# Kernel tuning notes

Hardware: AMD Instinct MI355X
Metric: run time of the kernel (lower is better)

Reference implementation:

```python
import jax, jax.numpy as jnp
import numpy as np

D_IN, HID, HEADS, MAXN, OUT, B = 16, 128, 4, 8, 128, 32768
HD = HID // HEADS
EPS = 1e-5


def _ln(x, g, b):
    m = jnp.mean(x, -1, keepdims=True)
    v = jnp.mean((x - m) ** 2, -1, keepdims=True)
    return (x - m) * jax.lax.rsqrt(v + EPS) * g + b


def _encode(x, enc_w1, enc_b1, enc_g1, enc_be1, enc_w2, enc_b2, enc_g2, enc_be2):
    h = _ln(x @ enc_w1.T + enc_b1, enc_g1, enc_be1)
    h = jax.nn.relu(h)
    return _ln(h @ enc_w2.T + enc_b2, enc_g2, enc_be2)


def setup_inputs() -> dict:
    key = jax.random.key(0)
    ks = jax.random.split(key, 12)

    def xavier(k, shape):
        # xavier_uniform with gain=0.5, matching _init_weights
        lim = 0.5 * np.sqrt(6.0 / (shape[0] + shape[1]))
        return jax.random.uniform(k, shape, jnp.float32, -lim, lim)

    z = lambda n: jnp.zeros((n,), jnp.float32)
    o = lambda n: jnp.ones((n,), jnp.float32)
    return {
        "current_node": jax.random.normal(ks[0], (B, D_IN), jnp.float32),
        "neighbor_nodes": jax.random.normal(ks[1], (B, MAXN, D_IN), jnp.float32),
        "neighbor_mask": jax.random.randint(ks[2], (B, MAXN), 0, 2, jnp.int32),
        "enc_w1": xavier(ks[3], (HID, D_IN)), "enc_b1": z(HID),
        "enc_g1": o(HID), "enc_be1": z(HID),
        "enc_w2": xavier(ks[4], (HID, HID)), "enc_b2": z(HID),
        "enc_g2": o(HID), "enc_be2": z(HID),
        "in_proj_w": xavier(ks[5], (3 * HID, HID)), "in_proj_b": z(3 * HID),
        "out_w": xavier(ks[6], (HID, HID)), "out_b": z(HID),
        "an_g": o(HID), "an_b": z(HID),
        "p1_w": xavier(ks[7], (HID, 2 * HID)), "p1_b": z(HID),
        "p1_g": o(HID), "p1_be": z(HID),
        "p2_w": xavier(ks[8], (OUT, HID)), "p2_b": z(OUT),
        "p2_g": o(OUT), "p2_be": z(OUT),
    }


def _forward(current_node, neighbor_nodes, neighbor_mask,
             enc_w1, enc_b1, enc_g1, enc_be1, enc_w2, enc_b2, enc_g2, enc_be2,
             in_proj_w, in_proj_b, out_w, out_b, an_g, an_b,
             p1_w, p1_b, p1_g, p1_be, p2_w, p2_b, p2_g, p2_be):
    bsz = current_node.shape[0]
    cur_emb = _encode(current_node, enc_w1, enc_b1, enc_g1, enc_be1,
                      enc_w2, enc_b2, enc_g2, enc_be2)                  # [B, HID]
    nb_emb = _encode(neighbor_nodes, enc_w1, enc_b1, enc_g1, enc_be1,
                     enc_w2, enc_b2, enc_g2, enc_be2)                   # [B, N, HID]

    valid = neighbor_mask > 0                                            # [B, N]
    has_nb = jnp.any(valid, axis=1)                                      # [B]

    # MultiheadAttention (eval mode, dropout inactive): q from current node, k/v from neighbors
    wq, wk, wv = in_proj_w[:HID], in_proj_w[HID:2 * HID], in_proj_w[2 * HID:]
    bq, bk, bv = in_proj_b[:HID], in_proj_b[HID:2 * HID], in_proj_b[2 * HID:]
    q = (cur_emb @ wq.T + bq).reshape(bsz, HEADS, HD)                    # [B, H, hd]
    k = (nb_emb @ wk.T + bk).reshape(bsz, MAXN, HEADS, HD)               # [B, N, H, hd]
    v = (nb_emb @ wv.T + bv).reshape(bsz, MAXN, HEADS, HD)

    scores = jnp.einsum('bhd,bnhd->bhn', q, k) / np.sqrt(HD)             # [B, H, N]
    # rows with zero valid neighbors get a fully-open mask to avoid NaN softmax;
    # their attention result is discarded below (replaced by cur_emb)
    safe = jnp.where(has_nb[:, None], valid, True)                       # [B, N]
    scores = jnp.where(safe[:, None, :], scores, -1e9)
    attn = jax.nn.softmax(scores, axis=-1)                               # [B, H, N]
    ctx = jnp.einsum('bhn,bnhd->bhd', attn, v).reshape(bsz, HID)
    ctx = ctx @ out_w.T + out_b
    agg = jnp.where(has_nb[:, None], _ln(ctx, an_g, an_b), cur_emb)      # [B, HID]

    combined = jnp.concatenate([cur_emb, agg], axis=-1)                  # [B, 2*HID]
    h = _ln(combined @ p1_w.T + p1_b, p1_g, p1_be)
    h = jax.nn.relu(h)
    return _ln(h @ p2_w.T + p2_b, p2_g, p2_be)                           # [B, OUT]


def reference(current_node, neighbor_nodes, neighbor_mask,
              enc_w1, enc_b1, enc_g1, enc_be1, enc_w2, enc_b2, enc_g2, enc_be2,
              in_proj_w, in_proj_b, out_w, out_b, an_g, an_b,
              p1_w, p1_b, p1_g, p1_be, p2_w, p2_b, p2_g, p2_be):
    return _forward(current_node, neighbor_nodes, neighbor_mask,
                    enc_w1, enc_b1, enc_g1, enc_be1, enc_w2, enc_b2, enc_g2, enc_be2,
                    in_proj_w, in_proj_b, out_w, out_b, an_g, an_b,
                    p1_w, p1_b, p1_g, p1_be, p2_w, p2_b, p2_g, p2_be)
```

## Files before the change

### kernel.cpp

```cpp
#include <hip/hip_runtime.h>

#define DEV __device__ __forceinline__

typedef __attribute__((ext_vector_type(8))) short bf16x8;
typedef __attribute__((ext_vector_type(4))) float f32x4;

static constexpr int NTH = 512;
static constexpr int TBE = 16;

static constexpr int W1P = 0;
static constexpr int W2  = 4096;
static constexpr int WQ  = 20480;
static constexpr int WK  = 36864;
static constexpr int WVW = 53248;
static constexpr int OW  = 69632;
static constexpr int P1A = 86016;
static constexpr int P1B = 102400;
static constexpr int P2W = 118784;
static constexpr int WS_BF16_TOT = 135168;
static constexpr int NPRM = 18 * 128;
static constexpr int WQr  = 139776;
static constexpr int OWr  = 156160;
static constexpr int P1Ar = 172544;
static constexpr int P1Br = 188928;
static constexpr int P2r  = 205312;
static constexpr int CURE = 221696;
static constexpr int NBE  = 221696 + 4194304;
static constexpr size_t SPLIT_NEED = (size_t)(NBE + 33554432) * 2;

DEV unsigned short f2bf(float f) {
  unsigned u = __float_as_uint(f);
  return (unsigned short)((u + 0x7fffu + ((u >> 16) & 1u)) >> 16);
}
DEV float bf2f(unsigned short u) { return __uint_as_float(((unsigned)u) << 16); }

DEV void st_bf16(unsigned short* buf, int row, int col, float v) {
  buf[row * 128 + ((((col >> 3) ^ (row & 7)) << 3) | (col & 7))] = f2bf(v);
}
DEV float ld_bf16(const unsigned short* buf, int row, int col) {
  unsigned u = buf[row * 128 + ((((col >> 3) ^ (row & 7)) << 3) | (col & 7))];
  return __uint_as_float(u << 16);
}
DEV bf16x8 frag128(const unsigned short* buf, int row, int kk, int lg) {
  return *(const bf16x8*)(buf + row * 128 + (((kk * 4 + lg) ^ (row & 7)) << 3));
}
DEV bf16x8 frag32(const unsigned short* buf, int row, int lg) {
  return *(const bf16x8*)(buf + row * 32 + ((lg ^ (row & 3)) << 3));
}
DEV f32x4 mfma16(bf16x8 a, bf16x8 b, f32x4 c) {
  return __builtin_amdgcn_mfma_f32_16x16x32_bf16(a, b, c, 0, 0, 0);
}

__global__ void prep(const float* __restrict__ enc_w1, const float* __restrict__ enc_w2,
                     const float* __restrict__ in_pw, const float* __restrict__ out_w,
                     const float* __restrict__ p1_w, const float* __restrict__ p2_w,
                     const float* __restrict__ enc_b1, const float* __restrict__ enc_g1,
                     const float* __restrict__ enc_be1, const float* __restrict__ enc_b2,
                     const float* __restrict__ enc_g2, const float* __restrict__ enc_be2,
                     const float* __restrict__ in_pb, const float* __restrict__ out_b,
                     const float* __restrict__ an_g, const float* __restrict__ an_b,
                     const float* __restrict__ p1_b, const float* __restrict__ p1_g,
                     const float* __restrict__ p1_be, const float* __restrict__ p2_b,
                     const float* __restrict__ p2_g, const float* __restrict__ p2_be,
                     unsigned short* __restrict__ wsb, float* __restrict__ wsp, int rm) {
  int t = blockIdx.x * blockDim.x + threadIdx.x;
  int NT = gridDim.x * blockDim.x;
  for (int i = t; i < 8 * 16384; i += NT) {
    int mi = i >> 14, e = i & 16383, row = e >> 7, col = e & 127;
    float v; int dstb;
    switch (mi) {
      case 0: v = enc_w2[row * 128 + col];         dstb = W2;  break;
      case 1: v = in_pw[row * 128 + col];          dstb = WQ;  break;
      case 2: v = in_pw[(128 + row) * 128 + col];  dstb = WK;  break;
      case 3: v = in_pw[(256 + row) * 128 + col];  dstb = WVW; break;
      case 4: v = out_w[row * 128 + col];          dstb = OW;  break;
      case 5: v = p1_w[row * 256 + col];           dstb = P1A; break;
      case 6: v = p1_w[row * 256 + 128 + col];     dstb = P1B; break;
      default: v = p2_w[row * 128 + col];          dstb = P2W; break;
    }
    wsb[dstb + row * 128 + ((((col >> 3) ^ (row & 7)) << 3) | (col & 7))] = f2bf(v);
  }
  for (int i = t; i < 4096; i += NT) {
    int row = i >> 5, col = i & 31;
    float v = (col < 16) ? enc_w1[row * 16 + col] : 0.f;
    wsb[W1P + row * 32 + ((((col >> 3) ^ (row & 3)) << 3) | (col & 7))] = f2bf(v);
  }
  if (rm) {
    for (int i = t; i < 5 * 16384; i += NT) {
      int mi = i >> 14, e = i & 16383, row = e >> 7, col = e & 127;
      float v; int dstb;
      switch (mi) {
        case 0: v = in_pw[row * 128 + col];         dstb = WQr;  break;
        case 1: v = out_w[row * 128 + col];         dstb = OWr;  break;
        case 2: v = p1_w[row * 256 + col];          dstb = P1Ar; break;
        case 3: v = p1_w[row * 256 + 128 + col];    dstb = P1Br; break;
        default: v = p2_w[row * 128 + col];         dstb = P2r;  break;
      }
      wsb[dstb + e] = f2bf(v);
    }
  }
  for (int i = t; i < NPRM; i += NT) {
    int s = i >> 7, c = i & 127; float v;
    switch (s) {
      case 0: v = enc_b1[c]; break;  case 1: v = enc_g1[c]; break;
      case 2: v = enc_be1[c]; break; case 3: v = enc_b2[c]; break;
      case 4: v = enc_g2[c]; break;  case 5: v = enc_be2[c]; break;
      case 6: v = in_pb[c]; break;   case 7: v = in_pb[128 + c]; break;
      case 8: v = in_pb[256 + c]; break; case 9: v = out_b[c]; break;
      case 10: v = an_g[c]; break;   case 11: v = an_b[c]; break;
      case 12: v = p1_b[c]; break;   case 13: v = p1_g[c]; break;
      case 14: v = p1_be[c]; break;  case 15: v = p2_b[c]; break;
      case 16: v = p2_g[c]; break;   default: v = p2_be[c]; break;
    }
    wsp[i] = v;
  }
}

__global__ __launch_bounds__(512, 4)
void k1_enc(const float* __restrict__ cur_x, const float* __restrict__ nb_x,
            const unsigned short* __restrict__ wsb, const float* __restrict__ wsp,
            unsigned short* __restrict__ wse) {
  __shared__ __align__(16) unsigned short s_w1[4096];
  __shared__ __align__(16) unsigned short s_w2[16384];
  __shared__ __align__(16) unsigned short s_h1[8][16 * 136];
  __shared__ float s_prm[6 * 128];

  const int tid = threadIdx.x;
  const int wv = tid >> 6, l = tid & 63, l15 = l & 15, lg = l >> 4;

  ((uint4*)s_w1)[tid] = ((const uint4*)(wsb + W1P))[tid];
#pragma unroll
  for (int i = 0; i < 4; ++i)
    ((uint4*)s_w2)[tid + i * 512] = ((const uint4*)(wsb + W2))[tid + i * 512];
  for (int i = tid; i < 768; i += 512) s_prm[i] = wsp[i];
  __syncthreads();

  unsigned short* h1 = &s_h1[wv][0];

  auto ln_t = [&](float (&acc)[8][4], int bs, int gs, int es, bool relu) {
#pragma unroll
    for (int ct = 0; ct < 8; ++ct) {
      float4 bb = *(const float4*)&s_prm[bs * 128 + ct * 16 + lg * 4];
      acc[ct][0] += bb.x; acc[ct][1] += bb.y; acc[ct][2] += bb.z; acc[ct][3] += bb.w;
    }
    float sm = 0.f, sq = 0.f;
#pragma unroll
    for (int ct = 0; ct < 8; ++ct)
#pragma unroll
      for (int r = 0; r < 4; ++r) { sm += acc[ct][r]; sq = fmaf(acc[ct][r], acc[ct][r], sq); }
    sm += __shfl_xor(sm, 16); sq += __shfl_xor(sq, 16);
    sm += __shfl_xor(sm, 32); sq += __shfl_xor(sq, 32);
    float mean = sm * 0.0078125f;
    float var = fmaf(sq, 0.0078125f, -mean * mean);
    float inv = rsqrtf(var + 1e-5f);
#pragma unroll
    for (int ct = 0; ct < 8; ++ct) {
      float4 gg = *(const float4*)&s_prm[gs * 128 + ct * 16 + lg * 4];
      float4 ee = *(const float4*)&s_prm[es * 128 + ct * 16 + lg * 4];
      float ga[4] = {gg.x, gg.y, gg.z, gg.w}, ea[4] = {ee.x, ee.y, ee.z, ee.w};
#pragma unroll
      for (int r = 0; r < 4; ++r) {
        float v = (acc[ct][r] - mean) * inv * ga[r] + ea[r];
        acc[ct][r] = relu ? fmaxf(v, 0.f) : v;
      }
    }
  };

#pragma unroll 1
  for (int t = blockIdx.x * 8 + wv; t < 18432; t += 9216) {
    asm volatile("s_waitcnt lgkmcnt(0)" ::: "memory");
    const bool isnb = t < 16384;
    const float* src = isnb ? nb_x + (size_t)t * 256
                            : cur_x + ((size_t)t - 16384) * 256;
    unsigned short* dst = wse + (isnb ? (size_t)NBE + (size_t)t * 2048
                                      : (size_t)CURE + ((size_t)t - 16384) * 2048);

    float4 fin = ((const float4*)src)[l];
    {
      uint2 u;
      u.x = (unsigned)f2bf(fin.x) | ((unsigned)f2bf(fin.y) << 16);
      u.y = (unsigned)f2bf(fin.z) | ((unsigned)f2bf(fin.w) << 16);
      *(uint2*)(h1 + (l >> 2) * 16 + (l & 3) * 4) = u;
    }
    bf16x8 bx = (bf16x8){0, 0, 0, 0, 0, 0, 0, 0};
    if (lg < 2) bx = *(const bf16x8*)(h1 + l15 * 16 + lg * 8);

    float acc[8][4];
#pragma unroll
    for (int ct = 0; ct < 8; ++ct) {
      f32x4 a = {0.f, 0.f, 0.f, 0.f};
      a = mfma16(frag32(s_w1, ct * 16 + l15, lg), bx, a);
      acc[ct][0] = a[0]; acc[ct][1] = a[1]; acc[ct][2] = a[2]; acc[ct][3] = a[3];
    }
    ln_t(acc, 0, 1, 2, true);
#pragma unroll
    for (int ct = 0; ct < 8; ++ct) {
      uint2 u;
      u.x = (unsigned)f2bf(acc[ct][0]) | ((unsigned)f2bf(acc[ct][1]) << 16);
      u.y = (unsigned)f2bf(acc[ct][2]) | ((unsigned)f2bf(acc[ct][3]) << 16);
      *(uint2*)(h1 + l15 * 136 + ct * 16 + lg * 4) = u;
    }

    bf16x8 bh[4];
#pragma unroll
    for (int kk = 0; kk < 4; ++kk)
      bh[kk] = *(const bf16x8*)(h1 + l15 * 136 + kk * 32 + lg * 8);
#pragma unroll
    for (int ct = 0; ct < 8; ++ct) {
      f32x4 a = {0.f, 0.f, 0.f, 0.f};
#pragma unroll
      for (int kk = 0; kk < 4; ++kk)
        a = mfma16(frag128(s_w2, ct * 16 + l15, kk, lg), bh[kk], a);
      acc[ct][0] = a[0]; acc[ct][1] = a[1]; acc[ct][2] = a[2]; acc[ct][3] = a[3];
    }
    ln_t(acc, 3, 4, 5, false);

#pragma unroll
    for (int ct = 0; ct < 8; ++ct) {
      uint2 u;
      u.x = (unsigned)f2bf(acc[ct][0]) | ((unsigned)f2bf(acc[ct][1]) << 16);
      u.y = (unsigned)f2bf(acc[ct][2]) | ((unsigned)f2bf(acc[ct][3]) << 16);
      int c = ct * 2 + (lg >> 1);
      *(uint2*)(h1 + l15 * 128 + ((c ^ l15) << 3) + (lg & 1) * 4) = u;
    }
#pragma unroll
    for (int i = 0; i < 4; ++i) {
      int R = i * 4 + lg;
      int j = l15;
      uint4 u = *(const uint4*)(h1 + R * 128 + ((j ^ R) << 3));
      ((uint4*)dst)[i * 64 + l] = u;
    }
  }
}

__global__ __launch_bounds__(256, 2)
void k2_head(const int* __restrict__ nb_mask,
             const unsigned short* __restrict__ wsb, const float* __restrict__ wsp,
             float* __restrict__ out) {
  __shared__ __align__(16) unsigned short s_stage[16384];
  __shared__ __align__(16) unsigned short s_q[16 * 136];
  __shared__ __align__(16) unsigned short s_cur[16 * 136];
  __shared__ __align__(16) unsigned short s_ctx[16 * 136];
  __shared__ __align__(16) unsigned short s_agg[16 * 136];
  __shared__ __align__(16) unsigned short s_hh[16 * 136];
  __shared__ __align__(16) float s_f[16 * 132];
  __shared__ __align__(16) float s_p[16 * 32];
  __shared__ float s_prm[NPRM];
  __shared__ int s_mask[16];

  const int tid = threadIdx.x;
  const int wv = tid >> 6, l = tid & 63, l15 = l & 15, lg = l >> 4;
  const int ebase = blockIdx.x * TBE;

  {
    int row = tid >> 4, chunk = tid & 15;
    ((uint4*)s_cur)[row * 17 + chunk] = ((const uint4*)(wsb + CURE))[(size_t)ebase * 16 + tid];
  }
  for (int i = tid; i < NPRM; i += 256) s_prm[i] = wsp[i];
  if (tid < 16) {
    int m = 0; const int* mp = nb_mask + (size_t)(ebase + tid) * 8;
#pragma unroll
    for (int n = 0; n < 8; ++n) m |= (mp[n] > 0) << n;
    s_mask[tid] = m;
  }
  __syncthreads();

  {
    bf16x8 a[4];
#pragma unroll
    for (int kk = 0; kk < 4; ++kk)
      a[kk] = *(const bf16x8*)(wsb + CURE + ((size_t)(ebase + l15)) * 128 + kk * 32 + lg * 8);
#pragma unroll
    for (int u = 0; u < 2; ++u) {
      int nt = wv * 2 + u;
      f32x4 acc = {0.f, 0.f, 0.f, 0.f};
#pragma unroll
      for (int kk = 0; kk < 4; ++kk) {
        bf16x8 b = *(const bf16x8*)(wsb + WQr + (nt * 16 + l15) * 128 + kk * 32 + lg * 8);
        acc = mfma16(a[kk], b, acc);
      }
      int c = nt * 16 + l15;
      float bq = s_prm[6 * 128 + c];
#pragma unroll
      for (int r = 0; r < 4; ++r)
        s_q[(lg * 4 + r) * 136 + c] = f2bf((acc[r] + bq) * 0.17677669529663687f);
    }
  }
#pragma unroll
  for (int i = 0; i < 8; ++i)
    ((uint4*)s_stage)[tid + i * 256] = ((const uint4*)(wsb + WK))[tid + i * 256];
  __syncthreads();

#pragma unroll 1
  for (int mi = 0; mi < 2; ++mi) {
    int mt = wv * 2 + mi;
    int el = mt * 2 + (lg >> 1);
    bf16x8 a[4];
#pragma unroll
    for (int kk = 0; kk < 4; ++kk)
      a[kk] = *(const bf16x8*)(wsb + NBE + ((size_t)ebase * 8 + mt * 16 + l15) * 128 + kk * 32 + lg * 8);
    float sacc[4][4];
#pragma unroll
    for (int h = 0; h < 4; ++h)
#pragma unroll
      for (int r = 0; r < 4; ++r) sacc[h][r] = 0.f;
#pragma unroll
    for (int nt = 0; nt < 8; ++nt) {
      f32x4 k4 = {0.f, 0.f, 0.f, 0.f};
#pragma unroll
      for (int kk = 0; kk < 4; ++kk)
        k4 = mfma16(a[kk], frag128(s_stage, nt * 16 + l15, kk, lg), k4);
      float qv = bf2f(s_q[el * 136 + nt * 16 + l15]);
      int h = nt >> 1;
#pragma unroll
      for (int r = 0; r < 4; ++r) sacc[h][r] = fmaf(k4[r], qv, sacc[h][r]);
    }
#pragma unroll
    for (int off = 1; off <= 8; off <<= 1)
#pragma unroll
      for (int h = 0; h < 4; ++h)
#pragma unroll
        for (int r = 0; r < 4; ++r) sacc[h][r] += __shfl_xor(sacc[h][r], off);
    int m = s_mask[el];
    int nbase = (lg & 1) * 4;
    float p[4][4];
#pragma unroll
    for (int h = 0; h < 4; ++h) {
      float mx = -1e30f;
#pragma unroll
      for (int r = 0; r < 4; ++r) {
        bool use = (m == 0) || ((m >> (nbase + r)) & 1);
        mx = fmaxf(mx, use ? sacc[h][r] : -1e30f);
      }
      mx = fmaxf(mx, __shfl_xor(mx, 16));
      float sum = 0.f;
#pragma unroll
      for (int r = 0; r < 4; ++r) {
        bool use = (m == 0) || ((m >> (nbase + r)) & 1);
        p[h][r] = use ? __expf(sacc[h][r] - mx) : 0.f;
        sum += p[h][r];
      }
      sum += __shfl_xor(sum, 16);
      float inv = 1.f / sum;
#pragma unroll
      for (int r = 0; r < 4; ++r) p[h][r] *= inv;
    }
    if (l15 == 0) {
#pragma unroll
      for (int h = 0; h < 4; ++h)
#pragma unroll
        for (int r = 0; r < 4; ++r) s_p[el * 32 + h * 8 + nbase + r] = p[h][r];
    }
  }
  __syncthreads();
#pragma unroll
  for (int i = 0; i < 8; ++i)
    ((uint4*)s_stage)[tid + i * 256] = ((const uint4*)(wsb + WVW))[tid + i * 256];
  __syncthreads();

#pragma unroll 1
  for (int mi = 0; mi < 2; ++mi) {
    int mt = wv * 2 + mi;
    int el = mt * 2 + (lg >> 1);
    bf16x8 a[4];
#pragma unroll
    for (int kk = 0; kk < 4; ++kk)
      a[kk] = *(const bf16x8*)(wsb + NBE + ((size_t)ebase * 8 + mt * 16 + l15) * 128 + kk * 32 + lg * 8);
    float4 p4[4];
#pragma unroll
    for (int h = 0; h < 4; ++h)
      p4[h] = *(const float4*)&s_p[el * 32 + h * 8 + (lg & 1) * 4];
    float cacc[8];
#pragma unroll
    for (int nt = 0; nt < 8; ++nt) {
      f32x4 v4 = {0.f, 0.f, 0.f, 0.f};
#pragma unroll
      for (int kk = 0; kk < 4; ++kk)
        v4 = mfma16(a[kk], frag128(s_stage, nt * 16 + l15, kk, lg), v4);
      int h = nt >> 1;
      cacc[nt] = p4[h].x * v4[0] + p4[h].y * v4[1] + p4[h].z * v4[2] + p4[h].w * v4[3];
    }
#pragma unroll
    for (int nt = 0; nt < 8; ++nt) cacc[nt] += __shfl_xor(cacc[nt], 16);
    if ((lg & 1) == 0) {
#pragma unroll
      for (int nt = 0; nt < 8; ++nt) {
        int c = nt * 16 + l15;
        s_ctx[el * 136 + c] = f2bf(cacc[nt] + s_prm[8 * 128 + c]);
      }
    }
  }
  __syncthreads();

  {
    bf16x8 a[4];
#pragma unroll
    for (int kk = 0; kk < 4; ++kk)
      a[kk] = *(const bf16x8*)(s_ctx + l15 * 136 + kk * 32 + lg * 8);
#pragma unroll
    for (int u = 0; u < 2; ++u) {
      int nt = wv * 2 + u;
      f32x4 acc = {0.f, 0.f, 0.f, 0.f};
#pragma unroll
      for (int kk = 0; kk < 4; ++kk) {
        bf16x8 b = *(const bf16x8*)(wsb + OWr + (nt * 16 + l15) * 128 + kk * 32 + lg * 8);
        acc = mfma16(a[kk], b, acc);
      }
      int c = nt * 16 + l15;
      float bo = s_prm[9 * 128 + c];
#pragma unroll
      for (int r = 0; r < 4; ++r) s_f[(lg * 4 + r) * 132 + c] = acc[r] + bo;
    }
  }
  __syncthreads();

  {
    int eo = wv * 4 + (l >> 4);
    float4 x0 = *(const float4*)&s_f[eo * 132 + l15 * 8];
    float4 x1 = *(const float4*)&s_f[eo * 132 + l15 * 8 + 4];
    float xa[8] = {x0.x, x0.y, x0.z, x0.w, x1.x, x1.y, x1.z, x1.w};
    float sm = 0.f, sq = 0.f;
#pragma unroll
    for (int j = 0; j < 8; ++j) { sm += xa[j]; sq = fmaf(xa[j], xa[j], sq); }
#pragma unroll
    for (int off = 1; off <= 8; off <<= 1) { sm += __shfl_xor(sm, off); sq += __shfl_xor(sq, off); }
    float mean = sm * 0.0078125f;
    float var = fmaf(sq, 0.0078125f, -mean * mean);
    float inv = rsqrtf(var + 1e-5f);
    int m = s_mask[eo];
    unsigned short o8[8];
    const unsigned short* cu = s_cur + eo * 136 + l15 * 8;
#pragma unroll
    for (int j = 0; j < 8; ++j) {
      int c = l15 * 8 + j;
      float v = (xa[j] - mean) * inv * s_prm[10 * 128 + c] + s_prm[11 * 128 + c];
      o8[j] = m ? f2bf(v) : cu[j];
    }
    uint4 u;
    u.x = (unsigned)o8[0] | ((unsigned)o8[1] << 16);
    u.y = (unsigned)o8[2] | ((unsigned)o8[3] << 16);
    u.z = (unsigned)o8[4] | ((unsigned)o8[5] << 16);
    u.w = (unsigned)o8[6] | ((unsigned)o8[7] << 16);
    *(uint4*)(s_agg + eo * 136 + l15 * 8) = u;
  }
  __syncthreads();

  {
    bf16x8 ac[4], ag[4];
#pragma unroll
    for (int kk = 0; kk < 4; ++kk) {
      ac[kk] = *(const bf16x8*)(s_cur + l15 * 136 + kk * 32 + lg * 8);
      ag[kk] = *(const bf16x8*)(s_agg + l15 * 136 + kk * 32 + lg * 8);
    }
#pragma unroll
    for (int u = 0; u < 2; ++u) {
      int nt = wv * 2 + u;
      f32x4 acc = {0.f, 0.f, 0.f, 0.f};
#pragma unroll
      for (int kk = 0; kk < 4; ++kk) {
        bf16x8 b = *(const bf16x8*)(wsb + P1Ar + (nt * 16 + l15) * 128 + kk * 32 + lg * 8);
        acc = mfma16(ac[kk], b, acc);
      }
#pragma unroll
      for (int kk = 0; kk < 4; ++kk) {
        bf16x8 b = *(const bf16x8*)(wsb + P1Br + (nt * 16 + l15) * 128 + kk * 32 + lg * 8);
        acc = mfma16(ag[kk], b, acc);
      }
      int c = nt * 16 + l15;
      float bb = s_prm[12 * 128 + c];
#pragma unroll
      for (int r = 0; r < 4; ++r) s_f[(lg * 4 + r) * 132 + c] = acc[r] + bb;
    }
  }
  __syncthreads();

  {
    int eo = wv * 4 + (l >> 4);
    float4 x0 = *(const float4*)&s_f[eo * 132 + l15 * 8];
    float4 x1 = *(const float4*)&s_f[eo * 132 + l15 * 8 + 4];
    float xa[8] = {x0.x, x0.y, x0.z, x0.w, x1.x, x1.y, x1.z, x1.w};
    float sm = 0.f, sq = 0.f;
#pragma unroll
    for (int j = 0; j < 8; ++j) { sm += xa[j]; sq = fmaf(xa[j], xa[j], sq); }
#pragma unroll
    for (int off = 1; off <= 8; off <<= 1) { sm += __shfl_xor(sm, off); sq += __shfl_xor(sq, off); }
    float mean = sm * 0.0078125f;
    float var = fmaf(sq, 0.0078125f, -mean * mean);
    float inv = rsqrtf(var + 1e-5f);
    unsigned short o8[8];
#pragma unroll
    for (int j = 0; j < 8; ++j) {
      int c = l15 * 8 + j;
      float v = (xa[j] - mean) * inv * s_prm[13 * 128 + c] + s_prm[14 * 128 + c];
      o8[j] = f2bf(fmaxf(v, 0.f));
    }
    uint4 u;
    u.x = (unsigned)o8[0] | ((unsigned)o8[1] << 16);
    u.y = (unsigned)o8[2] | ((unsigned)o8[3] << 16);
    u.z = (unsigned)o8[4] | ((unsigned)o8[5] << 16);
    u.w = (unsigned)o8[6] | ((unsigned)o8[7] << 16);
    *(uint4*)(s_hh + eo * 136 + l15 * 8) = u;
  }
  __syncthreads();

  {
    bf16x8 a[4];
#pragma unroll
    for (int kk = 0; kk < 4; ++kk)
      a[kk] = *(const bf16x8*)(s_hh + l15 * 136 + kk * 32 + lg * 8);
#pragma unroll
    for (int u = 0; u < 2; ++u) {
      int nt = wv * 2 + u;
      f32x4 acc = {0.f, 0.f, 0.f, 0.f};
#pragma unroll
      for (int kk = 0; kk < 4; ++kk) {
        bf16x8 b = *(const bf16x8*)(wsb + P2r + (nt * 16 + l15) * 128 + kk * 32 + lg * 8);
        acc = mfma16(a[kk], b, acc);
      }
      int c = nt * 16 + l15;
      float bb = s_prm[15 * 128 + c];
#pragma unroll
      for (int r = 0; r < 4; ++r) s_f[(lg * 4 + r) * 132 + c] = acc[r] + bb;
    }
  }
  __syncthreads();

  {
    int eo = wv * 4 + (l >> 4);
    float4 x0 = *(const float4*)&s_f[eo * 132 + l15 * 8];
    float4 x1 = *(const float4*)&s_f[eo * 132 + l15 * 8 + 4];
    float xa[8] = {x0.x, x0.y, x0.z, x0.w, x1.x, x1.y, x1.z, x1.w};
    float sm = 0.f, sq = 0.f;
#pragma unroll
    for (int j = 0; j < 8; ++j) { sm += xa[j]; sq = fmaf(xa[j], xa[j], sq); }
#pragma unroll
    for (int off = 1; off <= 8; off <<= 1) { sm += __shfl_xor(sm, off); sq += __shfl_xor(sq, off); }
    float mean = sm * 0.0078125f;
    float var = fmaf(sq, 0.0078125f, -mean * mean);
    float inv = rsqrtf(var + 1e-5f);
    float o[8];
#pragma unroll
    for (int j = 0; j < 8; ++j) {
      int c = l15 * 8 + j;
      o[j] = (xa[j] - mean) * inv * s_prm[16 * 128 + c] + s_prm[17 * 128 + c];
    }
    float* op = out + (size_t)(ebase + eo) * 128 + l15 * 8;
    *(float4*)op = make_float4(o[0], o[1], o[2], o[3]);
    *(float4*)(op + 4) = make_float4(o[4], o[5], o[6], o[7]);
  }
}

__global__ __launch_bounds__(NTH, 1)
void gcn_mfma(const float* __restrict__ cur_x, const float* __restrict__ nb_x,
              const int* __restrict__ nb_mask,
              const unsigned short* __restrict__ wsb, const float* __restrict__ wsp,
              float* __restrict__ out) {
  __shared__ __align__(16) unsigned short s_stage[20480];
  __shared__ __align__(16) unsigned short s_X[144 * 32];
  __shared__ __align__(16) unsigned short s_H[144 * 128];
  __shared__ __align__(16) unsigned short s_Enb[128 * 128];
  __shared__ __align__(16) unsigned short s_Ecur[16 * 128];
  __shared__ __align__(16) float s_q[16 * 132];
  __shared__ __align__(16) float s_p[16 * 32];
  __shared__ __align__(16) unsigned short s_ctx[16 * 128];
  __shared__ __align__(16) unsigned short s_agg[16 * 128];
  __shared__ __align__(16) unsigned short s_hh[16 * 128];
  __shared__ float s_prm[NPRM];
  __shared__ int s_mask[16];

  const int tid = threadIdx.x;
  const int wv = tid >> 6, l = tid & 63, l15 = l & 15, lg = l >> 4;
  const int sub = l >> 5, l32 = l & 31;
  const int ebase = blockIdx.x * TBE;
  const int eo = wv * 2 + sub;

  auto stage = [&](int srcOff) {
    const uint4* s = (const uint4*)(wsb + srcOff);
    uint4* d = (uint4*)s_stage;
#pragma unroll
    for (int i = 0; i < 4; ++i) d[tid + i * NTH] = s[tid + i * NTH];
  };
  auto ln_epi = [&](float (&vals)[8][4], int bslot, int gslot, int beslot, bool relu) {
    float sm[4] = {0, 0, 0, 0}, sq[4] = {0, 0, 0, 0};
#pragma unroll
    for (int nt = 0; nt < 8; ++nt) {
      float b = s_prm[bslot * 128 + nt * 16 + l15];
#pragma unroll
      for (int r = 0; r < 4; ++r) {
        float v = vals[nt][r] + b; vals[nt][r] = v;
        sm[r] += v; sq[r] = fmaf(v, v, sq[r]);
      }
    }
#pragma unroll
    for (int off = 8; off >= 1; off >>= 1)
#pragma unroll
      for (int r = 0; r < 4; ++r) {
        sm[r] += __shfl_xor(sm[r], off);
        sq[r] += __shfl_xor(sq[r], off);
      }
    float mean[4], inv[4];
#pragma unroll
    for (int r = 0; r < 4; ++r) {
      mean[r] = sm[r] * 0.0078125f;
      float var = fmaf(sq[r], 0.0078125f, -mean[r] * mean[r]);
      inv[r] = rsqrtf(var + 1e-5f);
    }
#pragma unroll
    for (int nt = 0; nt < 8; ++nt) {
      int col = nt * 16 + l15;
      float g = s_prm[gslot * 128 + col], be = s_prm[beslot * 128 + col];
#pragma unroll
      for (int r = 0; r < 4; ++r) {
        float v = (vals[nt][r] - mean[r]) * inv[r] * g + be;
        vals[nt][r] = relu ? fmaxf(v, 0.f) : v;
      }
    }
  };

  {
    const uint4* s = (const uint4*)(wsb + W1P);
    ((uint4*)(s_stage + 16384))[tid] = s[tid];
  }
  for (int i = tid; i < NPRM; i += NTH) s_prm[i] = wsp[i];
  for (int i = tid; i < 4608; i += NTH) {
    int row = i >> 5, col = i & 31;
    int e = (row * 57) >> 9, kind = row - e * 9;
    float v = 0.f;
    if (col < 16) {
      int ge = ebase + e;
      v = (kind == 0) ? cur_x[(size_t)ge * 16 + col]
                      : nb_x[((size_t)ge * 8 + (kind - 1)) * 16 + col];
// ... 224 lines not shown
    for (int c = 0; c < 4; ++c) {
      int col = l32 * 4 + c;
      r4[c] = fmaxf((xa[c] - mean) * inv * s_prm[13 * 128 + col] + s_prm[14 * 128 + col], 0.f);
    }
    uint2 uu;
    uu.x = (unsigned)f2bf(r4[0]) | ((unsigned)f2bf(r4[1]) << 16);
    uu.y = (unsigned)f2bf(r4[2]) | ((unsigned)f2bf(r4[3]) << 16);
    *(uint2*)(s_hh + eo * 128 + (((l32 >> 1) ^ (eo & 7)) << 3) + (l32 & 1) * 4) = uu;
  }
  __syncthreads();

  {
    f32x4 acc = {0.f, 0.f, 0.f, 0.f};
#pragma unroll
    for (int kk = 0; kk < 4; ++kk)
      acc = mfma16(frag128(s_hh, l15, kk, lg), frag128(s_stage, wv * 16 + l15, kk, lg), acc);
    int col = wv * 16 + l15; float b = s_prm[15 * 128 + col];
#pragma unroll
    for (int r = 0; r < 4; ++r) s_q[(lg * 4 + r) * 132 + col] = acc[r] + b;
  }
  __syncthreads();

  {
    float4 x = *(const float4*)&s_q[eo * 132 + l32 * 4];
    float s = x.x + x.y + x.z + x.w;
    float qq = fmaf(x.x, x.x, fmaf(x.y, x.y, fmaf(x.z, x.z, x.w * x.w)));
#pragma unroll
    for (int off = 16; off >= 1; off >>= 1) { s += __shfl_xor(s, off); qq += __shfl_xor(qq, off); }
    float mean = s * 0.0078125f;
    float var = fmaf(qq, 0.0078125f, -mean * mean);
    float inv = rsqrtf(var + 1e-5f);
    float xa[4] = {x.x, x.y, x.z, x.w};
    float4 o;
    o.x = (xa[0] - mean) * inv * s_prm[16 * 128 + l32 * 4 + 0] + s_prm[17 * 128 + l32 * 4 + 0];
    o.y = (xa[1] - mean) * inv * s_prm[16 * 128 + l32 * 4 + 1] + s_prm[17 * 128 + l32 * 4 + 1];
    o.z = (xa[2] - mean) * inv * s_prm[16 * 128 + l32 * 4 + 2] + s_prm[17 * 128 + l32 * 4 + 2];
    o.w = (xa[3] - mean) * inv * s_prm[16 * 128 + l32 * 4 + 3] + s_prm[17 * 128 + l32 * 4 + 3];
    *(float4*)&out[(size_t)(ebase + eo) * 128 + l32 * 4] = o;
  }
}

extern "C" void kernel_launch(void* const* d_in, const int* in_sizes, int n_in,
                              void* d_out, int out_size, void* d_ws, size_t ws_size,
                              hipStream_t stream) {
  const float* cur_x   = (const float*)d_in[0];
  const float* nb_x    = (const float*)d_in[1];
  const int*   nbm     = (const int*)d_in[2];
  const float* enc_w1  = (const float*)d_in[3];
  const float* enc_b1  = (const float*)d_in[4];
  const float* enc_g1  = (const float*)d_in[5];
  const float* enc_be1 = (const float*)d_in[6];
  const float* enc_w2  = (const float*)d_in[7];
  const float* enc_b2  = (const float*)d_in[8];
  const float* enc_g2  = (const float*)d_in[9];
  const float* enc_be2 = (const float*)d_in[10];
  const float* in_pw   = (const float*)d_in[11];
  const float* in_pb   = (const float*)d_in[12];
  const float* out_w   = (const float*)d_in[13];
  const float* out_b   = (const float*)d_in[14];
  const float* an_g    = (const float*)d_in[15];
  const float* an_b    = (const float*)d_in[16];
  const float* p1_w    = (const float*)d_in[17];
  const float* p1_b    = (const float*)d_in[18];
  const float* p1_g    = (const float*)d_in[19];
  const float* p1_be   = (const float*)d_in[20];
  const float* p2_w    = (const float*)d_in[21];
  const float* p2_b    = (const float*)d_in[22];
  const float* p2_g    = (const float*)d_in[23];
  const float* p2_be   = (const float*)d_in[24];
  float* out = (float*)d_out;

  unsigned short* wsb = (unsigned short*)d_ws;
  float* wsp = (float*)(wsb + WS_BF16_TOT);
  const int B = in_sizes[0] / 16;
  const bool split = (ws_size >= SPLIT_NEED) && (B == 32768);

  prep<<<128, 256, 0, stream>>>(enc_w1, enc_w2, in_pw, out_w, p1_w, p2_w,
                                enc_b1, enc_g1, enc_be1, enc_b2, enc_g2, enc_be2,
                                in_pb, out_b, an_g, an_b, p1_b, p1_g, p1_be,
                                p2_b, p2_g, p2_be, wsb, wsp, split ? 1 : 0);

  if (split) {
    k1_enc<<<1152, 512, 0, stream>>>(cur_x, nb_x, wsb, wsp, wsb);
    k2_head<<<B / TBE, 256, 0, stream>>>(nbm, wsb, wsp, out);
  } else {
    gcn_mfma<<<B / TBE, NTH, 0, stream>>>(cur_x, nb_x, nbm, wsb, wsp, out);
  }
}
```

Measured before the change: 137.2 us.

## Restructure attention head per-wave with K-projection folded into query

Rewrites the head kernel so each wave independently processes 16 elements, removing the block-wide __syncthreads between stages. Attention scores are computed by projecting q through W_k transposed (q·Wk) and dotting directly with neighbor embeddings, and the context is formed as an attention-weighted sum of neighbor embeddings before a single V projection. This avoids projecting K and V for all 8 neighbors. It adds a transposed Wk copy in prep and more scalar FMA work on VALU, and it drops the K bias term, which cancels in softmax.

```diff
diff --git a/kernel.cpp b/kernel.cpp
--- a/kernel.cpp
+++ b/kernel.cpp
@@ -24,8 +24,9 @@
 static constexpr int P1Ar = 172544;
 static constexpr int P1Br = 188928;
 static constexpr int P2r  = 205312;
-static constexpr int CURE = 221696;
-static constexpr int NBE  = 221696 + 4194304;
+static constexpr int WKt  = 221696;
+static constexpr int CURE = 238080;
+static constexpr int NBE  = 238080 + 4194304;
 static constexpr size_t SPLIT_NEED = (size_t)(NBE + 33554432) * 2;
 
 DEV unsigned short f2bf(float f) {
@@ -86,7 +87,7 @@
     wsb[W1P + row * 32 + ((((col >> 3) ^ (row & 3)) << 3) | (col & 7))] = f2bf(v);
   }
   if (rm) {
-    for (int i = t; i < 5 * 16384; i += NT) {
+    for (int i = t; i < 6 * 16384; i += NT) {
       int mi = i >> 14, e = i & 16383, row = e >> 7, col = e & 127;
       float v; int dstb;
       switch (mi) {
@@ -94,7 +95,8 @@
         case 1: v = out_w[row * 128 + col];         dstb = OWr;  break;
         case 2: v = p1_w[row * 256 + col];          dstb = P1Ar; break;
         case 3: v = p1_w[row * 256 + 128 + col];    dstb = P1Br; break;
-        default: v = p2_w[row * 128 + col];         dstb = P2r;  break;
+        case 4: v = p2_w[row * 128 + col];          dstb = P2r;  break;
+        default: v = in_pw[(128 + col) * 128 + row]; dstb = WKt; break;
       }
       wsb[dstb + e] = f2bf(v);
     }
@@ -237,316 +239,300 @@
 void k2_head(const int* __restrict__ nb_mask,
              const unsigned short* __restrict__ wsb, const float* __restrict__ wsp,
              float* __restrict__ out) {
-  __shared__ __align__(16) unsigned short s_stage[16384];
-  __shared__ __align__(16) unsigned short s_q[16 * 136];
-  __shared__ __align__(16) unsigned short s_cur[16 * 136];
-  __shared__ __align__(16) unsigned short s_ctx[16 * 136];
-  __shared__ __align__(16) unsigned short s_agg[16 * 136];
-  __shared__ __align__(16) unsigned short s_hh[16 * 136];
-  __shared__ __align__(16) float s_f[16 * 132];
-  __shared__ __align__(16) float s_p[16 * 32];
+  __shared__ __align__(16) unsigned short s_buf[4][3][16 * 136];
   __shared__ float s_prm[NPRM];
-  __shared__ int s_mask[16];
+  __shared__ int s_mask[64];
 
   const int tid = threadIdx.x;
   const int wv = tid >> 6, l = tid & 63, l15 = l & 15, lg = l >> 4;
-  const int ebase = blockIdx.x * TBE;
-
-  {
-    int row = tid >> 4, chunk = tid & 15;
-    ((uint4*)s_cur)[row * 17 + chunk] = ((const uint4*)(wsb + CURE))[(size_t)ebase * 16 + tid];
-  }
+  const int ew = (blockIdx.x * 4 + wv) * 16;
+  unsigned short* bufA = &s_buf[wv][0][0];
+  unsigned short* bufB = &s_buf[wv][1][0];
+  unsigned short* bufC = &s_buf[wv][2][0];
+
   for (int i = tid; i < NPRM; i += 256) s_prm[i] = wsp[i];
-  if (tid < 16) {
-    int m = 0; const int* mp = nb_mask + (size_t)(ebase + tid) * 8;
+  {
+    const uint4* src = (const uint4*)(wsb + CURE + (size_t)ew * 128);
+#pragma unroll
+    for (int i = 0; i < 4; ++i) {
+      int idx = i * 64 + l, row = idx >> 4, ch = idx & 15;
+      *(uint4*)(bufA + row * 136 + ch * 8) = src[idx];
+    }
+  }
+  if (l < 16) {
+    int m = 0; const int* mp = nb_mask + (size_t)(ew + l) * 8;
 #pragma unroll
     for (int n = 0; n < 8; ++n) m |= (mp[n] > 0) << n;
-    s_mask[tid] = m;
-  }
-  __syncthreads();
-
-  {
-    bf16x8 a[4];
-#pragma unroll
-    for (int kk = 0; kk < 4; ++kk)
-      a[kk] = *(const bf16x8*)(wsb + CURE + ((size_t)(ebase + l15)) * 128 + kk * 32 + lg * 8);
-#pragma unroll
-    for (int u = 0; u < 2; ++u) {
-      int nt = wv * 2 + u;
-      f32x4 acc = {0.f, 0.f, 0.f, 0.f};
-#pragma unroll
-      for (int kk = 0; kk < 4; ++kk) {
-        bf16x8 b = *(const bf16x8*)(wsb + WQr + (nt * 16 + l15) * 128 + kk * 32 + lg * 8);
-        acc = mfma16(a[kk], b, acc);
-      }
-      int c = nt * 16 + l15;
-      float bq = s_prm[6 * 128 + c];
-#pragma unroll
-      for (int r = 0; r < 4; ++r)
-        s_q[(lg * 4 + r) * 136 + c] = f2bf((acc[r] + bq) * 0.17677669529663687f);
-    }
-  }
-#pragma unroll
-  for (int i = 0; i < 8; ++i)
-    ((uint4*)s_stage)[tid + i * 256] = ((const uint4*)(wsb + WK))[tid + i * 256];
-  __syncthreads();
-
-#pragma unroll 1
-  for (int mi = 0; mi < 2; ++mi) {
-    int mt = wv * 2 + mi;
-    int el = mt * 2 + (lg >> 1);
-    bf16x8 a[4];
-#pragma unroll
-    for (int kk = 0; kk < 4; ++kk)
-      a[kk] = *(const bf16x8*)(wsb + NBE + ((size_t)ebase * 8 + mt * 16 + l15) * 128 + kk * 32 + lg * 8);
-    float sacc[4][4];
-#pragma unroll
-    for (int h = 0; h < 4; ++h)
-#pragma unroll
-      for (int r = 0; r < 4; ++r) sacc[h][r] = 0.f;
-#pragma unroll
-    for (int nt = 0; nt < 8; ++nt) {
-      f32x4 k4 = {0.f, 0.f, 0.f, 0.f};
-#pragma unroll
-      for (int kk = 0; kk < 4; ++kk)
-        k4 = mfma16(a[kk], frag128(s_stage, nt * 16 + l15, kk, lg), k4);
-      float qv = bf2f(s_q[el * 136 + nt * 16 + l15]);
-      int h = nt >> 1;
-#pragma unroll
-      for (int r = 0; r < 4; ++r) sacc[h][r] = fmaf(k4[r], qv, sacc[h][r]);
-    }
-#pragma unroll
-    for (int off = 1; off <= 8; off <<= 1)
-#pragma unroll
-      for (int h = 0; h < 4; ++h)
-#pragma unroll
-        for (int r = 0; r < 4; ++r) sacc[h][r] += __shfl_xor(sacc[h][r], off);
-    int m = s_mask[el];
-    int nbase = (lg & 1) * 4;
-    float p[4][4];
-#pragma unroll
-    for (int h = 0; h < 4; ++h) {
-      float mx = -1e30f;
-#pragma unroll
-      for (int r = 0; r < 4; ++r) {
-        bool use = (m == 0) || ((m >> (nbase + r)) & 1);
-        mx = fmaxf(mx, use ? sacc[h][r] : -1e30f);
-      }
-      mx = fmaxf(mx, __shfl_xor(mx, 16));
-      float sum = 0.f;
-#pragma unroll
-      for (int r = 0; r < 4; ++r) {
-        bool use = (m == 0) || ((m >> (nbase + r)) & 1);
-        p[h][r] = use ? __expf(sacc[h][r] - mx) : 0.f;
-        sum += p[h][r];
-      }
-      sum += __shfl_xor(sum, 16);
-      float inv = 1.f / sum;
-#pragma unroll
-      for (int r = 0; r < 4; ++r) p[h][r] *= inv;
-    }
-    if (l15 == 0) {
-#pragma unroll
-      for (int h = 0; h < 4; ++h)
-#pragma unroll
-        for (int r = 0; r < 4; ++r) s_p[el * 32 + h * 8 + nbase + r] = p[h][r];
-    }
-  }
-  __syncthreads();
-#pragma unroll
-  for (int i = 0; i < 8; ++i)
-    ((uint4*)s_stage)[tid + i * 256] = ((const uint4*)(wsb + WVW))[tid + i * 256];
-  __syncthreads();
-
-#pragma unroll 1
-  for (int mi = 0; mi < 2; ++mi) {
-    int mt = wv * 2 + mi;
-    int el = mt * 2 + (lg >> 1);
-    bf16x8 a[4];
-#pragma unroll
-    for (int kk = 0; kk < 4; ++kk)
-      a[kk] = *(const bf16x8*)(wsb + NBE + ((size_t)ebase * 8 + mt * 16 + l15) * 128 + kk * 32 + lg * 8);
-    float4 p4[4];
-#pragma unroll
-    for (int h = 0; h < 4; ++h)
-      p4[h] = *(const float4*)&s_p[el * 32 + h * 8 + (lg & 1) * 4];
-    float cacc[8];
-#pragma unroll
-    for (int nt = 0; nt < 8; ++nt) {
-      f32x4 v4 = {0.f, 0.f, 0.f, 0.f};
-#pragma unroll
-      for (int kk = 0; kk < 4; ++kk)
-        v4 = mfma16(a[kk], frag128(s_stage, nt * 16 + l15, kk, lg), v4);
-      int h = nt >> 1;
-      cacc[nt] = p4[h].x * v4[0] + p4[h].y * v4[1] + p4[h].z * v4[2] + p4[h].w * v4[3];
-    }
-#pragma unroll
-    for (int nt = 0; nt < 8; ++nt) cacc[nt] += __shfl_xor(cacc[nt], 16);
-    if ((lg & 1) == 0) {
-#pragma unroll
-      for (int nt = 0; nt < 8; ++nt) {
-        int c = nt * 16 + l15;
-        s_ctx[el * 136 + c] = f2bf(cacc[nt] + s_prm[8 * 128 + c]);
-      }
-    }
-  }
-  __syncthreads();
-
-  {
-    bf16x8 a[4];
-#pragma unroll
-    for (int kk = 0; kk < 4; ++kk)
-      a[kk] = *(const bf16x8*)(s_ctx + l15 * 136 + kk * 32 + lg * 8);
-#pragma unroll
-    for (int u = 0; u < 2; ++u) {
-      int nt = wv * 2 + u;
-      f32x4 acc = {0.f, 0.f, 0.f, 0.f};
-#pragma unroll
-      for (int kk = 0; kk < 4; ++kk) {
-        bf16x8 b = *(const bf16x8*)(wsb + OWr + (nt * 16 + l15) * 128 + kk * 32 + lg * 8);
-        acc = mfma16(a[kk], b, acc);
-      }
-      int c = nt * 16 + l15;
-      float bo = s_prm[9 * 128 + c];
-#pragma unroll
-      for (int r = 0; r < 4; ++r) s_f[(lg * 4 + r) * 132 + c] = acc[r] + bo;
-    }
-  }
-  __syncthreads();
-
-  {
-    int eo = wv * 4 + (l >> 4);
-    float4 x0 = *(const float4*)&s_f[eo * 132 + l15 * 8];
-    float4 x1 = *(const float4*)&s_f[eo * 132 + l15 * 8 + 4];
-    float xa[8] = {x0.x, x0.y, x0.z, x0.w, x1.x, x1.y, x1.z, x1.w};
+    s_mask[wv * 16 + l] = m;
+  }
+  __syncthreads();
+
+  float acc[8][4];
+
+  auto ln_t = [&](int bs, int gs, int es, bool relu) {
+#pragma unroll
+    for (int ct = 0; ct < 8; ++ct) {
+      float4 bb = *(const float4*)&s_prm[bs * 128 + ct * 16 + lg * 4];
+      acc[ct][0] += bb.x; acc[ct][1] += bb.y; acc[ct][2] += bb.z; acc[ct][3] += bb.w;
+    }
     float sm = 0.f, sq = 0.f;
 #pragma unroll
-    for (int j = 0; j < 8; ++j) { sm += xa[j]; sq = fmaf(xa[j], xa[j], sq); }
-#pragma unroll
-    for (int off = 1; off <= 8; off <<= 1) { sm += __shfl_xor(sm, off); sq += __shfl_xor(sq, off); }
+    for (int ct = 0; ct < 8; ++ct)
+#pragma unroll
+      for (int r = 0; r < 4; ++r) { sm += acc[ct][r]; sq = fmaf(acc[ct][r], acc[ct][r], sq); }
+    sm += __shfl_xor(sm, 16); sq += __shfl_xor(sq, 16);
+    sm += __shfl_xor(sm, 32); sq += __shfl_xor(sq, 32);
     float mean = sm * 0.0078125f;
     float var = fmaf(sq, 0.0078125f, -mean * mean);
     float inv = rsqrtf(var + 1e-5f);
-    int m = s_mask[eo];
-    unsigned short o8[8];
-    const unsigned short* cu = s_cur + eo * 136 + l15 * 8;
-#pragma unroll
-    for (int j = 0; j < 8; ++j) {
-      int c = l15 * 8 + j;
-      float v = (xa[j] - mean) * inv * s_prm[10 * 128 + c] + s_prm[11 * 128 + c];
-      o8[j] = m ? f2bf(v) : cu[j];
-    }
-    uint4 u;
-    u.x = (unsigned)o8[0] | ((unsigned)o8[1] << 16);
-    u.y = (unsigned)o8[2] | ((unsigned)o8[3] << 16);
-    u.z = (unsigned)o8[4] | ((unsigned)o8[5] << 16);
-    u.w = (unsigned)o8[6] | ((unsigned)o8[7] << 16);
-    *(uint4*)(s_agg + eo * 136 + l15 * 8) = u;
-  }
-  __syncthreads();
-
-  {
-    bf16x8 ac[4], ag[4];
+#pragma unroll
+    for (int ct = 0; ct < 8; ++ct) {
+      float4 gg = *(const float4*)&s_prm[gs * 128 + ct * 16 + lg * 4];
+      float4 ee = *(const float4*)&s_prm[es * 128 + ct * 16 + lg * 4];
+      float ga[4] = {gg.x, gg.y, gg.z, gg.w}, ea[4] = {ee.x, ee.y, ee.z, ee.w};
+#pragma unroll
+      for (int r = 0; r < 4; ++r) {
+        float v = (acc[ct][r] - mean) * inv * ga[r] + ea[r];
+        acc[ct][r] = relu ? fmaxf(v, 0.f) : v;
+      }
+    }
+  };
+
+  {
+    bf16x8 b[4];
+#pragma unroll
+    for (int kk = 0; kk < 4; ++kk) b[kk] = *(const bf16x8*)(bufA + l15 * 136 + kk * 32 + lg * 8);
+#pragma unroll
+    for (int ct = 0; ct < 8; ++ct) {
+      f32x4 a4 = {0.f, 0.f, 0.f, 0.f};
+#pragma unroll
+      for (int kk = 0; kk < 4; ++kk) {
+        bf16x8 w = *(const bf16x8*)(wsb + WQr + (ct * 16 + l15) * 128 + kk * 32 + lg * 8);
+        a4 = mfma16(w, b[kk], a4);
+      }
+      float4 bb = *(const float4*)&s_prm[6 * 128 + ct * 16 + lg * 4];
+      uint2 u;
+      u.x = (unsigned)f2bf((a4[0] + bb.x) * 0.17677669529663687f)
+          | ((unsigned)f2bf((a4[1] + bb.y) * 0.17677669529663687f) << 16);
+      u.y = (unsigned)f2bf((a4[2] + bb.z) * 0.17677669529663687f)
+          | ((unsigned)f2bf((a4[3] + bb.w) * 0.17677669529663687f) << 16);
+      *(uint2*)(bufB + l15 * 136 + ct * 16 + lg * 4) = u;
+    }
+  }
+  __builtin_amdgcn_sched_barrier(0);
+
+  bf16x8 qf[4][4];
+#pragma unroll
+  for (int h = 0; h < 4; ++h) {
+    bf16x8 qb = *(const bf16x8*)(bufB + l15 * 136 + h * 32 + lg * 8);
+    __builtin_amdgcn_sched_barrier(0);
+#pragma unroll
+    for (int ct = 0; ct < 8; ++ct) {
+      bf16x8 w = *(const bf16x8*)(wsb + WKt + (ct * 16 + l15) * 128 + h * 32 + lg * 8);
+      f32x4 a4 = {0.f, 0.f, 0.f, 0.f};
+      a4 = mfma16(w, qb, a4);
+      uint2 u;
+      u.x = (unsigned)f2bf(a4[0]) | ((unsigned)f2bf(a4[1]) << 16);
+      u.y = (unsigned)f2bf(a4[2]) | ((unsigned)f2bf(a4[3]) << 16);
+      *(uint2*)(bufC + l15 * 136 + ct * 16 + lg * 4) = u;
+    }
+    __builtin_amdgcn_sched_barrier(0);
+#pragma unroll
+    for (int kk = 0; kk < 4; ++kk)
+      qf[h][kk] = *(const bf16x8*)(bufC + l15 * 136 + kk * 32 + lg * 8);
+    __builtin_amdgcn_sched_barrier(0);
+  }
+
+  float pe[4][8];
+  {
+    const unsigned short* nbp = wsb + NBE + (size_t)(ew + l15) * 1024;
+    float ps[4][8];
+#pragma unroll
+    for (int h = 0; h < 4; ++h)
+#pragma unroll
+      for (int n = 0; n < 8; ++n) ps[h][n] = 0.f;
+#pragma unroll
+    for (int n = 0; n < 8; ++n) {
+#pragma unroll
+      for (int kk = 0; kk < 4; ++kk) {
+        bf16x8 nf = *(const bf16x8*)(nbp + n * 128 + kk * 32 + lg * 8);
+#pragma unroll
+        for (int i = 0; i < 8; ++i) {
+          float nv = bf2f((unsigned short)nf[i]);
+          ps[0][n] = fmaf(nv, bf2f((unsigned short)qf[0][kk][i]), ps[0][n]);
+          ps[1][n] = fmaf(nv, bf2f((unsigned short)qf[1][kk][i]), ps[1][n]);
+          ps[2][n] = fmaf(nv, bf2f((unsigned short)qf[2][kk][i]), ps[2][n]);
+          ps[3][n] = fmaf(nv, bf2f((unsigned short)qf[3][kk][i]), ps[3][n]);
+        }
+      }
+    }
+#pragma unroll
+    for (int h = 0; h < 4; ++h)
+#pragma unroll
+      for (int n = 0; n < 8; ++n) {
+        ps[h][n] += __shfl_xor(ps[h][n], 16);
+        ps[h][n] += __shfl_xor(ps[h][n], 32);
+      }
+    int m = s_mask[wv * 16 + l15];
+    bool all = (m == 0);
+#pragma unroll
+    for (int h = 0; h < 4; ++h) {
+      float mx = -1e30f;
+#pragma unroll
+      for (int n = 0; n < 8; ++n) {
+        bool u = all || ((m >> n) & 1);
+        mx = fmaxf(mx, u ? ps[h][n] : -1e30f);
+      }
+      float su = 0.f;
+#pragma unroll
+      for (int n = 0; n < 8; ++n) {
+        bool u = all || ((m >> n) & 1);
+        pe[h][n] = u ? __expf(ps[h][n] - mx) : 0.f;
+        su += pe[h][n];
+      }
+      float inv = 1.f / su;
+#pragma unroll
+      for (int n = 0; n < 8; ++n) pe[h][n] *= inv;
+    }
+  }
+  __builtin_amdgcn_sched_barrier(0);
+
+  {
+    const unsigned short* nbp = wsb + NBE + (size_t)(ew + l15) * 1024;
+#pragma unroll
+    for (int h = 0; h < 4; ++h) {
+      float pn[4][8];
+#pragma unroll
+      for (int kk = 0; kk < 4; ++kk)
+#pragma unroll
+        for (int i = 0; i < 8; ++i) pn[kk][i] = 0.f;
+#pragma unroll
+      for (int n = 0; n < 8; ++n) {
+        float pv = pe[h][n];
+#pragma unroll
+        for (int kk = 0; kk < 4; ++kk) {
+          bf16x8 nf = *(const bf16x8*)(nbp + n * 128 + kk * 32 + lg * 8);
+#pragma unroll
+          for (int i = 0; i < 8; ++i)
+            pn[kk][i] = fmaf(bf2f((unsigned short)nf[i]), pv, pn[kk][i]);
+        }
+      }
+#pragma unroll
+      for (int kk = 0; kk < 4; ++kk) {
+        uint4 u;
+        u.x = (unsigned)f2bf(pn[kk][0]) | ((unsigned)f2bf(pn[kk][1]) << 16);
+        u.y = (unsigned)f2bf(pn[kk][2]) | ((unsigned)f2bf(pn[kk][3]) << 16);
+        u.z = (unsigned)f2bf(pn[kk][4]) | ((unsigned)f2bf(pn[kk][5]) << 16);
+        u.w = (unsigned)f2bf(pn[kk][6]) | ((unsigned)f2bf(pn[kk][7]) << 16);
+        *(uint4*)(bufC + l15 * 136 + kk * 32 + lg * 8) = u;
+      }
+      __builtin_amdgcn_sched_barrier(0);
+#pragma unroll
+      for (int cc = 0; cc < 2; ++cc) {
+        int ct = h * 2 + cc;
+        f32x4 a4 = {0.f, 0.f, 0.f, 0.f};
+#pragma unroll
+        for (int kk = 0; kk < 4; ++kk) {
+          bf16x8 b = *(const bf16x8*)(bufC + l15 * 136 + kk * 32 + lg * 8);
+          a4 = mfma16(frag128(wsb + WVW, ct * 16 + l15, kk, lg), b, a4);
+        }
+        float4 bb = *(const float4*)&s_prm[8 * 128 + ct * 16 + lg * 4];
+        uint2 u;
+        u.x = (unsigned)f2bf(a4[0] + bb.x) | ((unsigned)f2bf(a4[1] + bb.y) << 16);
+        u.y = (unsigned)f2bf(a4[2] + bb.z) | ((unsigned)f2bf(a4[3] + bb.w) << 16);
+        *(uint2*)(bufB + l15 * 136 + ct * 16 + lg * 4) = u;
+      }
+      __builtin_amdgcn_sched_barrier(0);
+    }
+  }
+
+  {
+    bf16x8 b[4];
+#pragma unroll
+    for (int kk = 0; kk < 4; ++kk) b[kk] = *(const bf16x8*)(bufB + l15 * 136 + kk * 32 + lg * 8);
+    __builtin_amdgcn_sched_barrier(0);
+#pragma unroll
+    for (int ct = 0; ct < 8; ++ct) {
+      f32x4 a4 = {0.f, 0.f, 0.f, 0.f};
+#pragma unroll
+      for (int kk = 0; kk < 4; ++kk) {
+        bf16x8 w = *(const bf16x8*)(wsb + OWr + (ct * 16 + l15) * 128 + kk * 32 + lg * 8);
+        a4 = mfma16(w, b[kk], a4);
+      }
+      acc[ct][0] = a4[0]; acc[ct][1] = a4[1]; acc[ct][2] = a4[2]; acc[ct][3] = a4[3];
+    }
+    ln_t(9, 10, 11, false);
+    int m = s_mask[wv * 16 + l15];
+#pragma unroll
+    for (int ct = 0; ct < 8; ++ct) {
+      uint2 cu = *(const uint2*)(bufA + l15 * 136 + ct * 16 + lg * 4);
+      unsigned short a0 = m ? f2bf(acc[ct][0]) : (unsigned short)(cu.x & 0xffff);
+      unsigned short a1 = m ? f2bf(acc[ct][1]) : (unsigned short)(cu.x >> 16);
+      unsigned short a2 = m ? f2bf(acc[ct][2]) : (unsigned short)(cu.y & 0xffff);
+      unsigned short a3 = m ? f2bf(acc[ct][3]) : (unsigned short)(cu.y >> 16);
+      uint2 u;
+      u.x = (unsigned)a0 | ((unsigned)a1 << 16);
+      u.y = (unsigned)a2 | ((unsigned)a3 << 16);
+      *(uint2*)(bufB + l15 * 136 + ct * 16 + lg * 4) = u;
+    }
+  }
+  __builtin_amdgcn_sched_barrier(0);
+
+  {
+    bf16x8 bc[4], bg[4];
 #pragma unroll
     for (int kk = 0; kk < 4; ++kk) {
-      ac[kk] = *(const bf16x8*)(s_cur + l15 * 136 + kk * 32 + lg * 8);
-      ag[kk] = *(const bf16x8*)(s_agg + l15 * 136 + kk * 32 + lg * 8);
-    }
-#pragma unroll
-    for (int u = 0; u < 2; ++u) {
-      int nt = wv * 2 + u;
-      f32x4 acc = {0.f, 0.f, 0.f, 0.f};
+      bc[kk] = *(const bf16x8*)(bufA + l15 * 136 + kk * 32 + lg * 8);
+      bg[kk] = *(const bf16x8*)(bufB + l15 * 136 + kk * 32 + lg * 8);
+    }
+    __builtin_amdgcn_sched_barrier(0);
+#pragma unroll
+    for (int ct = 0; ct < 8; ++ct) {
+      f32x4 a4 = {0.f, 0.f, 0.f, 0.f};
 #pragma unroll
       for (int kk = 0; kk < 4; ++kk) {
-        bf16x8 b = *(const bf16x8*)(wsb + P1Ar + (nt * 16 + l15) * 128 + kk * 32 + lg * 8);
-        acc = mfma16(ac[kk], b, acc);
+        bf16x8 w = *(const bf16x8*)(wsb + P1Ar + (ct * 16 + l15) * 128 + kk * 32 + lg * 8);
+        a4 = mfma16(w, bc[kk], a4);
       }
 #pragma unroll
       for (int kk = 0; kk < 4; ++kk) {
-        bf16x8 b = *(const bf16x8*)(wsb + P1Br + (nt * 16 + l15) * 128 + kk * 32 + lg * 8);
-        acc = mfma16(ag[kk], b, acc);
-      }
-      int c = nt * 16 + l15;
-      float bb = s_prm[12 * 128 + c];
-#pragma unroll
-      for (int r = 0; r < 4; ++r) s_f[(lg * 4 + r) * 132 + c] = acc[r] + bb;
-    }
-  }
-  __syncthreads();
-
-  {
-    int eo = wv * 4 + (l >> 4);
-    float4 x0 = *(const float4*)&s_f[eo * 132 + l15 * 8];
-    float4 x1 = *(const float4*)&s_f[eo * 132 + l15 * 8 + 4];
-    float xa[8] = {x0.x, x0.y, x0.z, x0.w, x1.x, x1.y, x1.z, x1.w};
-    float sm = 0.f, sq = 0.f;
-#pragma unroll
-    for (int j = 0; j < 8; ++j) { sm += xa[j]; sq = fmaf(xa[j], xa[j], sq); }
-#pragma unroll
-    for (int off = 1; off <= 8; off <<= 1) { sm += __shfl_xor(sm, off); sq += __shfl_xor(sq, off); }
-    float mean = sm * 0.0078125f;
-    float var = fmaf(sq, 0.0078125f, -mean * mean);
-    float inv = rsqrtf(var + 1e-5f);
-    unsigned short o8[8];
-#pragma unroll
-    for (int j = 0; j < 8; ++j) {
-      int c = l15 * 8 + j;
-      float v = (xa[j] - mean) * inv * s_prm[13 * 128 + c] + s_prm[14 * 128 + c];
-      o8[j] = f2bf(fmaxf(v, 0.f));
-    }
-    uint4 u;
-    u.x = (unsigned)o8[0] | ((unsigned)o8[1] << 16);
-    u.y = (unsigned)o8[2] | ((unsigned)o8[3] << 16);
-    u.z = (unsigned)o8[4] | ((unsigned)o8[5] << 16);
-    u.w = (unsigned)o8[6] | ((unsigned)o8[7] << 16);
-    *(uint4*)(s_hh + eo * 136 + l15 * 8) = u;
-  }
-  __syncthreads();
-
-  {
-    bf16x8 a[4];
-#pragma unroll
-    for (int kk = 0; kk < 4; ++kk)
-      a[kk] = *(const bf16x8*)(s_hh + l15 * 136 + kk * 32 + lg * 8);
-#pragma unroll
-    for (int u = 0; u < 2; ++u) {
-      int nt = wv * 2 + u;
-      f32x4 acc = {0.f, 0.f, 0.f, 0.f};
+        bf16x8 w = *(const bf16x8*)(wsb + P1Br + (ct * 16 + l15) * 128 + kk * 32 + lg * 8);
+        a4 = mfma16(w, bg[kk], a4);
+      }
+      acc[ct][0] = a4[0]; acc[ct][1] = a4[1]; acc[ct][2] = a4[2]; acc[ct][3] = a4[3];
+    }
+    ln_t(12, 13, 14, true);
+#pragma unroll
+    for (int ct = 0; ct < 8; ++ct) {
+      uint2 u;
+      u.x = (unsigned)f2bf(acc[ct][0]) | ((unsigned)f2bf(acc[ct][1]) << 16);
+      u.y = (unsigned)f2bf(acc[ct][2]) | ((unsigned)f2bf(acc[ct][3]) << 16);
+      *(uint2*)(bufB + l15 * 136 + ct * 16 + lg * 4) = u;
+    }
+  }
+  __builtin_amdgcn_sched_barrier(0);
+
+  {
+    bf16x8 b[4];
+#pragma unroll
+    for (int kk = 0; kk < 4; ++kk) b[kk] = *(const bf16x8*)(bufB + l15 * 136 + kk * 32 + lg * 8);
+    __builtin_amdgcn_sched_barrier(0);
+#pragma unroll
+    for (int ct = 0; ct < 8; ++ct) {
+      f32x4 a4 = {0.f, 0.f, 0.f, 0.f};
 #pragma unroll
       for (int kk = 0; kk < 4; ++kk) {
-        bf16x8 b = *(const bf16x8*)(wsb + P2r + (nt * 16 + l15) * 128 + kk * 32 + lg * 8);
-        acc = mfma16(a[kk], b, acc);
-      }
-      int c = nt * 16 + l15;
-      float bb = s_prm[15 * 128 + c];
-#pragma unroll
-      for (int r = 0; r < 4; ++r) s_f[(lg * 4 + r) * 132 + c] = acc[r] + bb;
-    }
-  }
-  __syncthreads();
-
-  {
-    int eo = wv * 4 + (l >> 4);
-    float4 x0 = *(const float4*)&s_f[eo * 132 + l15 * 8];
-    float4 x1 = *(const float4*)&s_f[eo * 132 + l15 * 8 + 4];
-    float xa[8] = {x0.x, x0.y, x0.z, x0.w, x1.x, x1.y, x1.z, x1.w};
-    float sm = 0.f, sq = 0.f;
-#pragma unroll
-    for (int j = 0; j < 8; ++j) { sm += xa[j]; sq = fmaf(xa[j], xa[j], sq); }
-#pragma unroll
-    for (int off = 1; off <= 8; off <<= 1) { sm += __shfl_xor(sm, off); sq += __shfl_xor(sq, off); }
-    float mean = sm * 0.0078125f;
-    float var = fmaf(sq, 0.0078125f, -mean * mean);
-    float inv = rsqrtf(var + 1e-5f);
-    float o[8];
-#pragma unroll
-    for (int j = 0; j < 8; ++j) {
-      int c = l15 * 8 + j;
-      o[j] = (xa[j] - mean) * inv * s_prm[16 * 128 + c] + s_prm[17 * 128 + c];
-    }
-    float* op = out + (size_t)(ebase + eo) * 128 + l15 * 8;
-    *(float4*)op = make_float4(o[0], o[1], o[2], o[3]);
-    *(float4*)(op + 4) = make_float4(o[4], o[5], o[6], o[7]);
+        bf16x8 w = *(const bf16x8*)(wsb + P2r + (ct * 16 + l15) * 128 + kk * 32 + lg * 8);
+        a4 = mfma16(w, b[kk], a4);
+      }
+      acc[ct][0] = a4[0]; acc[ct][1] = a4[1]; acc[ct][2] = a4[2]; acc[ct][3] = a4[3];
+    }
+    ln_t(15, 16, 17, false);
+    float* op = out + (size_t)(ew + l15) * 128;
+#pragma unroll
+    for (int ct = 0; ct < 8; ++ct)
+      *(float4*)(op + ct * 16 + lg * 4) =
+          make_float4(acc[ct][0], acc[ct][1], acc[ct][2], acc[ct][3]);
   }
 }
 
@@ -937,7 +923,7 @@
 
   if (split) {
     k1_enc<<<1152, 512, 0, stream>>>(cur_x, nb_x, wsb, wsp, wsb);
-    k2_head<<<B / TBE, 256, 0, stream>>>(nbm, wsb, wsp, out);
+    k2_head<<<B / 64, 256, 0, stream>>>(nbm, wsb, wsp, out);
   } else {
     gcn_mfma<<<B / TBE, NTH, 0, stream>>>(cur_x, nb_x, nbm, wsb, wsp, out);
   }
```

Result: slower. 143.3 us (+4.5%).
